# Optimization experiments

Hardware: AMD Instinct MI355X
Metric: run time of the kernel (lower is better)

The kernel has to match this reference:

```python
import jax, jax.numpy as jnp
import numpy as np

B, S, HID = 2, 2048, 2048
NH = 16
QLR, KVLR = 1536, 512
DN, DR, DV = 128, 64, 128          # qk_nope_head_dim, qk_rope_head_dim, v_head_dim
DQK = DN + DR                      # 192
SCALE = DQK ** -0.5
EPS = 1e-6


def rmsnorm(x, w):
    return x * jax.lax.rsqrt(jnp.mean(x * x, axis=-1, keepdims=True) + EPS) * w


def rotate_half(x):
    h = x.shape[-1] // 2
    return jnp.concatenate([-x[..., h:], x[..., :h]], axis=-1)


def setup_inputs() -> dict:
    key = jax.random.key(0)
    k = jax.random.split(key, 8)
    hidden_states = jax.random.normal(k[0], (B, S, HID), jnp.float32)
    # additive causal mask [B,1,S,S]
    causal = jnp.tril(jnp.ones((S, S), bool))
    attention_mask = jnp.where(causal, 0.0, -1e9).astype(jnp.float32)[None, None]
    attention_mask = jnp.broadcast_to(attention_mask, (B, 1, S, S))
    # RoPE tables for the rope head dim
    inv_freq = 1.0 / (10000.0 ** (jnp.arange(0, DR, 2, dtype=jnp.float32) / DR))
    t = jnp.arange(S, dtype=jnp.float32)[:, None] * inv_freq[None, :]
    emb = jnp.concatenate([t, t], axis=-1)        # [S, DR]
    cos, sin = jnp.cos(emb), jnp.sin(emb)
    s = 0.02
    w_qa = jax.random.normal(k[1], (HID, QLR), jnp.float32) * s
    qa_ln = jnp.ones((QLR,), jnp.float32)
    w_qb = jax.random.normal(k[2], (QLR, NH * DQK), jnp.float32) * s
    w_kva = jax.random.normal(k[3], (HID, KVLR + DR), jnp.float32) * s
    kva_ln = jnp.ones((KVLR,), jnp.float32)
    w_kvb = jax.random.normal(k[4], (KVLR, NH * (DN + DV)), jnp.float32) * s
    w_o = jax.random.normal(k[5], (NH * DV, HID), jnp.float32) * s
    return {"hidden_states": hidden_states, "attention_mask": attention_mask,
            "cos": cos, "sin": sin, "w_qa": w_qa, "qa_ln": qa_ln, "w_qb": w_qb,
            "w_kva": w_kva, "kva_ln": kva_ln, "w_kvb": w_kvb, "w_o": w_o}


def reference(hidden_states, attention_mask, cos, sin, w_qa, qa_ln, w_qb,
              w_kva, kva_ln, w_kvb, w_o):
    b, s, _ = hidden_states.shape
    # q low-rank path: q_b_proj(q_a_layernorm(q_a_proj(x)))
    q = rmsnorm(hidden_states @ w_qa, qa_ln) @ w_qb            # [B,S,NH*DQK]
    q = q.reshape(b, s, NH, DQK).transpose(0, 2, 1, 3)          # [B,NH,S,DQK]
    q_nope, q_pe = q[..., :DN], q[..., DN:]
    # compressed kv + shared rope key
    ckv = hidden_states @ w_kva                                 # [B,S,KVLR+DR]
    k_c, k_pe = ckv[..., :KVLR], ckv[..., KVLR:]
    kv = rmsnorm(k_c, kva_ln) @ w_kvb                           # [B,S,NH*(DN+DV)]
    kv = kv.reshape(b, s, NH, DN + DV).transpose(0, 2, 1, 3)    # [B,NH,S,DN+DV]
    k_nope, value_states = kv[..., :DN], kv[..., DN:]
    # RoPE on rope dims (k_pe is MQA: one head)
    k_pe = k_pe.reshape(b, 1, s, DR)
    c = cos[None, None]  # [1,1,S,DR]
    si = sin[None, None]
    q_pe = q_pe * c + rotate_half(q_pe) * si
    k_pe = k_pe * c + rotate_half(k_pe) * si
    k_pe = jnp.broadcast_to(k_pe, (b, NH, s, DR))
    query_states = jnp.concatenate([q_nope, q_pe], axis=-1)     # [B,NH,S,DQK]
    key_states = jnp.concatenate([k_nope, k_pe], axis=-1)       # [B,NH,S,DQK]
    attn_weights = jnp.einsum('bhqd,bhkd->bhqk', query_states, key_states) * SCALE
    attn_weights = attn_weights + attention_mask
    attn_probs = jax.nn.softmax(attn_weights.astype(jnp.float32), axis=-1)
    attn_probs = attn_probs.astype(value_states.dtype)
    attn_output = jnp.einsum('bhqk,bhkd->bhqd', attn_probs, value_states)
    attn_output = attn_output.transpose(0, 2, 1, 3).reshape(b, s, NH * DV)
    return attn_output @ w_o                                    # [B,S,HID]
```

## Files before the change

kernel.cpp:

```cpp
#include <hip/hip_runtime.h>
#include <type_traits>

typedef __attribute__((ext_vector_type(8))) short  vshort8;
typedef __attribute__((ext_vector_type(8))) __bf16 vbf16x8;
typedef __attribute__((ext_vector_type(4))) float  vfloat4;

__device__ __forceinline__ float bf2f(unsigned short h) {
    return __uint_as_float(((unsigned int)h) << 16);
}
__device__ __forceinline__ unsigned short f2bf(float f) {
    unsigned int u = __float_as_uint(f);
    unsigned int r = (u + 0x7FFFu + ((u >> 16) & 1u)) >> 16;
    return (unsigned short)r;
}
__device__ __forceinline__ vshort8 cvt8(const float* p) {
    float4 a = *(const float4*)p;
    float4 b = *(const float4*)(p + 4);
    vshort8 r;
    r[0] = (short)f2bf(a.x); r[1] = (short)f2bf(a.y);
    r[2] = (short)f2bf(a.z); r[3] = (short)f2bf(a.w);
    r[4] = (short)f2bf(b.x); r[5] = (short)f2bf(b.y);
    r[6] = (short)f2bf(b.z); r[7] = (short)f2bf(b.w);
    return r;
}
__device__ __forceinline__ void gload16(const void* g, void* lds) {
    __builtin_amdgcn_global_load_lds(
        (const __attribute__((address_space(1))) unsigned int*)g,
        (__attribute__((address_space(3))) unsigned int*)lds, 16, 0, 0);
}

__global__ __launch_bounds__(256) void hconv_kernel(
    const float* __restrict__ in, unsigned short* __restrict__ out, int n8)
{
    int i = blockIdx.x * 256 + threadIdx.x;
    if (i < n8) *(vshort8*)(out + (size_t)i * 8) = cvt8(in + (size_t)i * 8);
}

__global__ __launch_bounds__(256) void wtrans_kernel(
    const float* __restrict__ W, unsigned short* __restrict__ Wt,
    int ldw, int ldt, int rowoff)
{
    __shared__ __align__(16) unsigned short Ls[64][72];
    const int t = threadIdx.x;
    const int n0 = blockIdx.x * 64, k0 = blockIdx.y * 64;
    const int rr = t >> 2, cc = t & 3;

    const float* src = W + (size_t)(k0 + rr) * ldw + n0 + cc * 16;
    *(vshort8*)&Ls[rr][cc * 16]     = cvt8(src);
    *(vshort8*)&Ls[rr][cc * 16 + 8] = cvt8(src + 8);
    __syncthreads();

    unsigned short* dst = Wt + (size_t)(rowoff + n0 + rr) * ldt + k0 + cc * 16;
    vshort8 v0, v1;
    #pragma unroll
    for (int j = 0; j < 8; ++j) {
        v0[j] = (short)Ls[cc * 16 + j][rr];
        v1[j] = (short)Ls[cc * 16 + 8 + j][rr];
    }
    *(vshort8*)dst = v0;
    *(vshort8*)(dst + 8) = v1;
}

template<typename CT>
__global__ __launch_bounds__(256) void gemm_tt(
    const unsigned short* __restrict__ A, const unsigned short* __restrict__ Bt,
    CT* __restrict__ C0, CT* __restrict__ C1,
    int K, int N, int nsplit, int ldc0, int ldc1)
{
    __shared__ __align__(16) unsigned short As[128 * 32];
    __shared__ __align__(16) unsigned short Bs[128 * 32];

    const int t = threadIdx.x, lane = t & 63, w = t >> 6;
    const int lm = lane & 15, quad = lane >> 4;
    const int wm = w >> 1, wn = w & 1;
    const int m0 = blockIdx.y * 128, n0 = blockIdx.x * 128;
    const int srow = lane >> 2, sseg = lane & 3;

    vfloat4 acc[4][4] = {};

    for (int k0 = 0; k0 < K; k0 += 32) {
        #pragma unroll
        for (int j = 0; j < 2; ++j) {
            int r = w * 32 + j * 16 + srow;
            gload16(A  + (size_t)(m0 + r) * K + k0 + sseg * 8, &As[(w * 2 + j) * 512]);
            gload16(Bt + (size_t)(n0 + r) * K + k0 + sseg * 8, &Bs[(w * 2 + j) * 512]);
        }
        __syncthreads();

        vbf16x8 af[4], bw[4];
        #pragma unroll
        for (int i = 0; i < 4; ++i) {
            af[i] = *(const vbf16x8*)&As[(wm * 64 + i * 16 + lm) * 32 + quad * 8];
            bw[i] = *(const vbf16x8*)&Bs[(wn * 64 + i * 16 + lm) * 32 + quad * 8];
        }
        #pragma unroll
        for (int mi = 0; mi < 4; ++mi)
            #pragma unroll
            for (int ni = 0; ni < 4; ++ni)
                acc[mi][ni] = __builtin_amdgcn_mfma_f32_16x16x32_bf16(af[mi], bw[ni], acc[mi][ni], 0, 0, 0);
        __syncthreads();
    }

    #pragma unroll
    for (int mi = 0; mi < 4; ++mi) {
        #pragma unroll
        for (int ni = 0; ni < 4; ++ni) {
            int col = n0 + wn * 64 + ni * 16 + lm;
            if (col >= N) continue;
            #pragma unroll
            for (int r = 0; r < 4; ++r) {
                int row = m0 + wm * 64 + mi * 16 + quad * 4 + r;
                float v = acc[mi][ni][r];
                if (col < nsplit) {
                    if constexpr (std::is_same_v<CT, float>) C0[(size_t)row * ldc0 + col] = v;
                    else C0[(size_t)row * ldc0 + col] = f2bf(v);
                } else {
                    if constexpr (std::is_same_v<CT, float>) C1[(size_t)row * ldc1 + col - nsplit] = v;
                    else C1[(size_t)row * ldc1 + col - nsplit] = f2bf(v);
                }
            }
        }
    }
}

__global__ __launch_bounds__(256) void gemm_kv(
    const unsigned short* __restrict__ A, const unsigned short* __restrict__ Bt,
    unsigned short* __restrict__ Kn, unsigned short* __restrict__ VT, int K)
{
    __shared__ __align__(16) unsigned short As[128 * 32];
    __shared__ __align__(16) unsigned short Bs[128 * 32];

    const int t = threadIdx.x, lane = t & 63, w = t >> 6;
    const int lm = lane & 15, quad = lane >> 4;
    const int wm = w >> 1, wn = w & 1;
    const int m0 = blockIdx.y * 128, n0 = blockIdx.x * 128;
    const int srow = lane >> 2, sseg = lane & 3;

    vfloat4 acc[4][4] = {};

    for (int k0 = 0; k0 < K; k0 += 32) {
        #pragma unroll
        for (int j = 0; j < 2; ++j) {
            int r = w * 32 + j * 16 + srow;
            gload16(A  + (size_t)(m0 + r) * K + k0 + sseg * 8, &As[(w * 2 + j) * 512]);
            gload16(Bt + (size_t)(n0 + r) * K + k0 + sseg * 8, &Bs[(w * 2 + j) * 512]);
        }
        __syncthreads();

        vbf16x8 af[4], bw[4];
        #pragma unroll
        for (int i = 0; i < 4; ++i) {
            af[i] = *(const vbf16x8*)&As[(wm * 64 + i * 16 + lm) * 32 + quad * 8];
            bw[i] = *(const vbf16x8*)&Bs[(wn * 64 + i * 16 + lm) * 32 + quad * 8];
        }
        #pragma unroll
        for (int mi = 0; mi < 4; ++mi)
            #pragma unroll
            for (int ni = 0; ni < 4; ++ni)
                acc[mi][ni] = __builtin_amdgcn_mfma_f32_16x16x32_bf16(af[mi], bw[ni], acc[mi][ni], 0, 0, 0);
        __syncthreads();
    }

    #pragma unroll
    for (int mi = 0; mi < 4; ++mi) {
        #pragma unroll
        for (int ni = 0; ni < 4; ++ni) {
            int col = n0 + wn * 64 + ni * 16 + lm;
            int h = col >> 8, d = col & 255;
            #pragma unroll
            for (int r = 0; r < 4; ++r) {
                int row = m0 + wm * 64 + mi * 16 + quad * 4 + r;
                float v = acc[mi][ni][r];
                if (d < 128) {
                    Kn[(size_t)row * 2048 + h * 128 + d] = f2bf(v);
                } else {
                    int b = row >> 11, tok = row & 2047;
                    VT[((size_t)(b * 16 + h) * 128 + d - 128) * 2048 + tok] = f2bf(v);
                }
            }
        }
    }
}

__global__ __launch_bounds__(256) void rmsnorm_kernel(
    const unsigned short* __restrict__ in, const float* __restrict__ wgt,
    unsigned short* __restrict__ out, int width, int ld_in, int ld_out)
{
    const int row = blockIdx.x;
    const int t = threadIdx.x;
    const unsigned short* x = in + (size_t)row * ld_in;

    float ss = 0.f;
    for (int i = t; i < width; i += 256) { float v = bf2f(x[i]); ss += v * v; }
    #pragma unroll
    for (int off = 32; off > 0; off >>= 1) ss += __shfl_down(ss, off, 64);

    __shared__ float red[4];
    __shared__ float rr;
    if ((t & 63) == 0) red[t >> 6] = ss;
    __syncthreads();
    if (t == 0) rr = rsqrtf((red[0] + red[1] + red[2] + red[3]) / (float)width + 1e-6f);
    __syncthreads();
    float r = rr;
    unsigned short* o = out + (size_t)row * ld_out;
    for (int i = t; i < width; i += 256) o[i] = f2bf(bf2f(x[i]) * r * wgt[i]);
}

__global__ __launch_bounds__(256) void rope_q_kernel(
    unsigned short* __restrict__ q, const float* __restrict__ cosb,
    const float* __restrict__ sinb)
{
    const int row = blockIdx.x;
    const int s = row & 2047;
    const int t = threadIdx.x;
    unsigned short* qr = q + (size_t)row * 3072;
    const float SCALE = 0.07216878364870323f;

    for (int c = t; c < 3072; c += 256) {
        int d = c % 192;
        if (d < 128) {
            qr[c] = f2bf(bf2f(qr[c]) * SCALE);
        } else if (d < 160) {
            int i = d - 128;
            float cs = cosb[s * 64 + i];
            float sn = sinb[s * 64 + i];
            float x = bf2f(qr[c]);
            float y = bf2f(qr[c + 32]);
            qr[c]      = f2bf((x * cs - y * sn) * SCALE);
            qr[c + 32] = f2bf((y * cs + x * sn) * SCALE);
        }
    }
}

__global__ __launch_bounds__(64) void rope_k_kernel(
    const unsigned short* __restrict__ ckv, const float* __restrict__ cosb,
    const float* __restrict__ sinb, unsigned short* __restrict__ kpe)
{
    const int row = blockIdx.x;
    const int s = row & 2047;
    const int t = threadIdx.x;
    if (t < 32) {
        float cs = cosb[s * 64 + t];
        float sn = sinb[s * 64 + t];
        float x = bf2f(ckv[(size_t)row * 576 + 512 + t]);
        float y = bf2f(ckv[(size_t)row * 576 + 544 + t]);
        kpe[(size_t)row * 64 + t]      = f2bf(x * cs - y * sn);
        kpe[(size_t)row * 64 + 32 + t] = f2bf(y * cs + x * sn);
    }
}

__global__ __launch_bounds__(256) void flash_kernel(
    const unsigned short* __restrict__ Q, const unsigned short* __restrict__ Kn,
    const unsigned short* __restrict__ KPE, const unsigned short* __restrict__ VT,
    unsigned short* __restrict__ O)
{
    __shared__ __align__(16) unsigned short Ks[64][200];
    __shared__ __align__(16) unsigned short Vs[128][72];
    __shared__ __align__(16) unsigned short Ps[4][16][72];

    const int t    = threadIdx.x;
    const int lane = t & 63;
    const int w    = t >> 6;
    const int lm   = lane & 15, quad = lane >> 4;
    const int h = blockIdx.y, b = blockIdx.z;
    const int tb = b * 2048;
    const unsigned short* VTbh = VT + (size_t)(b * 16 + h) * 128 * 2048;

    for (int pi = 0; pi < 2; ++pi) {
        const int qt = pi ? (31 - blockIdx.x) : blockIdx.x;

        const int qtok = tb + qt * 64 + w * 16 + lm;
        vbf16x8 aq[6];
        #pragma unroll
        for (int ch = 0; ch < 6; ++ch)
            aq[ch] = *(const vbf16x8*)(Q + (size_t)qtok * 3072 + h * 192 + ch * 32 + quad * 8);

        vfloat4 acc_o[8];
        #pragma unroll
        for (int i = 0; i < 8; ++i) acc_o[i] = (vfloat4){0, 0, 0, 0};
        float mrow[4], lrow[4];
        #pragma unroll
        for (int r = 0; r < 4; ++r) { mrow[r] = -3.0e38f; lrow[r] = 0.f; }

        for (int kt = 0; kt <= qt; ++kt) {
            const int kb = kt * 64;
            #pragma unroll
            for (int it = 0; it < 4; ++it) {
                int idx = t + it * 256;
                int row = idx >> 4, sg = idx & 15;
                *(vshort8*)&Ks[row][sg * 8] =
                    *(const vshort8*)(Kn + (size_t)(tb + kb + row) * 2048 + h * 128 + sg * 8);
            }
            #pragma unroll
            for (int it = 0; it < 2; ++it) {
                int idx = t + it * 256;
                int row = idx >> 3, sg = idx & 7;
                *(vshort8*)&Ks[row][128 + sg * 8] =
                    *(const vshort8*)(KPE + (size_t)(tb + kb + row) * 64 + sg * 8);
            }
            #pragma unroll
            for (int it = 0; it < 4; ++it) {
                int idx = t + it * 256;
                int d = idx >> 3, sg = idx & 7;
                *(vshort8*)&Vs[d][sg * 8] =
                    *(const vshort8*)(VTbh + (size_t)d * 2048 + kb + sg * 8);
            }
            __syncthreads();

            vfloat4 accs[4];
            #pragma unroll
            for (int ni = 0; ni < 4; ++ni) accs[ni] = (vfloat4){0, 0, 0, 0};
            #pragma unroll
            for (int ni = 0; ni < 4; ++ni) {
                #pragma unroll
                for (int ch = 0; ch < 6; ++ch) {
                    vbf16x8 bk = *(const vbf16x8*)&Ks[ni * 16 + lm][ch * 32 + quad * 8];
                    accs[ni] = __builtin_amdgcn_mfma_f32_16x16x32_bf16(aq[ch], bk, accs[ni], 0, 0, 0);
                }
            }

            const int qrow = qt * 64 + w * 16 + quad * 4;
            #pragma unroll
            for (int ni = 0; ni < 4; ++ni) {
                int ki = kb + ni * 16 + lm;
                #pragma unroll
                for (int r = 0; r < 4; ++r)
                    if (ki > qrow + r) accs[ni][r] = -3.0e38f;
            }

            #pragma unroll
            for (int r = 0; r < 4; ++r) {
                float mx = fmaxf(fmaxf(accs[0][r], accs[1][r]), fmaxf(accs[2][r], accs[3][r]));
                #pragma unroll
                for (int off = 1; off < 16; off <<= 1) mx = fmaxf(mx, __shfl_xor(mx, off, 64));
                float mnew  = fmaxf(mrow[r], mx);
                float alpha = __expf(mrow[r] - mnew);
                float sum = 0.f;
                #pragma unroll
                for (int ni = 0; ni < 4; ++ni) {
                    float pv = __expf(accs[ni][r] - mnew);
                    accs[ni][r] = pv;
                    sum += pv;
                }
                #pragma unroll
                for (int off = 1; off < 16; off <<= 1) sum += __shfl_xor(sum, off, 64);
                lrow[r] = lrow[r] * alpha + sum;
                mrow[r] = mnew;
                #pragma unroll
                for (int vt = 0; vt < 8; ++vt) acc_o[vt][r] *= alpha;
            }

            #pragma unroll
            for (int ni = 0; ni < 4; ++ni)
                #pragma unroll
                for (int r = 0; r < 4; ++r)
                    Ps[w][quad * 4 + r][ni * 16 + lm] = f2bf(accs[ni][r]);
            __syncthreads();

            #pragma unroll
            for (int kc = 0; kc < 2; ++kc) {
                vbf16x8 ap = *(const vbf16x8*)&Ps[w][lm][kc * 32 + quad * 8];
                #pragma unroll
                for (int vt = 0; vt < 8; ++vt) {
                    vbf16x8 bv = *(const vbf16x8*)&Vs[vt * 16 + lm][kc * 32 + quad * 8];
                    acc_o[vt] = __builtin_amdgcn_mfma_f32_16x16x32_bf16(ap, bv, acc_o[vt], 0, 0, 0);
                }
            }
            __syncthreads();
        }

        #pragma unroll
        for (int r = 0; r < 4; ++r) {
            float inv = 1.f / lrow[r];
            int tok = tb + qt * 64 + w * 16 + quad * 4 + r;
            #pragma unroll
            for (int vt = 0; vt < 8; ++vt)
                O[(size_t)tok * 2048 + h * 128 + vt * 16 + lm] = f2bf(acc_o[vt][r] * inv);
        }
    }
}

extern "C" void kernel_launch(void* const* d_in, const int* in_sizes, int n_in,
                              void* d_out, int out_size, void* d_ws, size_t ws_size,
                              hipStream_t stream) {
    const float* hidden = (const float*)d_in[0];
    const float* cosb   = (const float*)d_in[2];
    const float* sinb   = (const float*)d_in[3];
    const float* w_qa   = (const float*)d_in[4];
    const float* qa_ln  = (const float*)d_in[5];
    const float* w_qb   = (const float*)d_in[6];
    const float* w_kva  = (const float*)d_in[7];
    const float* kva_ln = (const float*)d_in[8];
    const float* w_kvb  = (const float*)d_in[9];
    const float* w_o    = (const float*)d_in[10];
    float* out = (float*)d_out;

    unsigned short* ws   = (unsigned short*)d_ws;
    unsigned short* hb   = ws;
    unsigned short* Kn   = ws;
    unsigned short* wt12 = ws + 8388608;
    unsigned short* VT   = ws + 8388608;
    unsigned short* ot   = ws + 8388608;
    unsigned short* qbuf = ws + 16777216;
    unsigned short* q_a  = ws + 29360128;
    unsigned short* ckv  = ws + 35651584;
    unsigned short* aout = ws + 29360128;
    unsigned short* qbt  = ws + 38010880;
    unsigned short* kvbt = ws + 42729472;
    unsigned short* kvn  = ws + 44826624;
    unsigned short* kpe  = ws + 46923776;

    dim3 blk(256);

    hconv_kernel<<<4096, blk, 0, stream>>>(hidden, hb, 1048576);
    wtrans_kernel<<<dim3(24, 32), blk, 0, stream>>>(w_qa,  wt12, 1536, 2048, 0);
    wtrans_kernel<<<dim3( 9, 32), blk, 0, stream>>>(w_kva, wt12,  576, 2048, 1536);
    wtrans_kernel<<<dim3(48, 24), blk, 0, stream>>>(w_qb,  qbt,  3072, 1536, 0);
    wtrans_kernel<<<dim3(64,  8), blk, 0, stream>>>(w_kvb, kvbt, 4096,  512, 0);

    gemm_tt<unsigned short><<<dim3(17, 32), blk, 0, stream>>>(
        hb, wt12, q_a, ckv, 2048, 2112, 1536, 1536, 576);

    rmsnorm_kernel<<<4096, blk, 0, stream>>>(q_a, qa_ln, q_a, 1536, 1536, 1536);
    rmsnorm_kernel<<<4096, blk, 0, stream>>>(ckv, kva_ln, kvn, 512, 576, 512);
    rope_k_kernel<<<4096, dim3(64), 0, stream>>>(ckv, cosb, sinb, kpe);

    gemm_tt<unsigned short><<<dim3(24, 32), blk, 0, stream>>>(
        q_a, qbt, qbuf, qbuf, 1536, 3072, 3072, 3072, 3072);
    rope_q_kernel<<<4096, blk, 0, stream>>>(qbuf, cosb, sinb);

    gemm_kv<<<dim3(32, 32), blk, 0, stream>>>(kvn, kvbt, Kn, VT, 512);

    flash_kernel<<<dim3(16, 16, 2), blk, 0, stream>>>(qbuf, Kn, kpe, VT, aout);

    wtrans_kernel<<<dim3(32, 32), blk, 0, stream>>>(w_o, ot, 2048, 2048, 0);

    gemm_tt<float><<<dim3(16, 32), blk, 0, stream>>>(
        aout, ot, out, out, 2048, 2048, 2048, 2048, 2048);
}
```

Before: 560.9 us.

## Prefetch next K/V tile into registers and launch one q-tile per block

The flash attention kernel now loads the next K, rope-K and V tile into registers while computing the current tile, then writes them to shared memory after the PV step, overlapping global loads with MFMA work. The paired-q-tile loop per block is replaced by one q-tile per block, with a doubled grid and heaviest tiles scheduled first. The causal mask is applied only on the diagonal tile, and launch bounds request 3 blocks per SM. This adds register pressure and an extra barrier per iteration, and balances load through hardware scheduling instead of manual pairing.

```diff
diff --git a/kernel.cpp b/kernel.cpp
--- a/kernel.cpp
+++ b/kernel.cpp
@@ -249,7 +249,7 @@
     }
 }
 
-__global__ __launch_bounds__(256) void flash_kernel(
+__global__ __launch_bounds__(256, 3) void flash_kernel(
     const unsigned short* __restrict__ Q, const unsigned short* __restrict__ Kn,
     const unsigned short* __restrict__ KPE, const unsigned short* __restrict__ VT,
     unsigned short* __restrict__ O)
@@ -265,60 +265,90 @@
     const int h = blockIdx.y, b = blockIdx.z;
     const int tb = b * 2048;
     const unsigned short* VTbh = VT + (size_t)(b * 16 + h) * 128 * 2048;
-
-    for (int pi = 0; pi < 2; ++pi) {
-        const int qt = pi ? (31 - blockIdx.x) : blockIdx.x;
-
-        const int qtok = tb + qt * 64 + w * 16 + lm;
-        vbf16x8 aq[6];
-        #pragma unroll
-        for (int ch = 0; ch < 6; ++ch)
-            aq[ch] = *(const vbf16x8*)(Q + (size_t)qtok * 3072 + h * 192 + ch * 32 + quad * 8);
-
-        vfloat4 acc_o[8];
-        #pragma unroll
-        for (int i = 0; i < 8; ++i) acc_o[i] = (vfloat4){0, 0, 0, 0};
-        float mrow[4], lrow[4];
-        #pragma unroll
-        for (int r = 0; r < 4; ++r) { mrow[r] = -3.0e38f; lrow[r] = 0.f; }
-
-        for (int kt = 0; kt <= qt; ++kt) {
-            const int kb = kt * 64;
+    const int qt = 31 - (int)blockIdx.x;
+
+    const int qtok = tb + qt * 64 + w * 16 + lm;
+    vbf16x8 aq[6];
+    #pragma unroll
+    for (int ch = 0; ch < 6; ++ch)
+        aq[ch] = *(const vbf16x8*)(Q + (size_t)qtok * 3072 + h * 192 + ch * 32 + quad * 8);
+
+    vfloat4 acc_o[8];
+    #pragma unroll
+    for (int i = 0; i < 8; ++i) acc_o[i] = (vfloat4){0, 0, 0, 0};
+    float mrow[4], lrow[4];
+    #pragma unroll
+    for (int r = 0; r < 4; ++r) { mrow[r] = -3.0e38f; lrow[r] = 0.f; }
+
+    vshort8 rk[4], rp[2], rv[4];
+
+    #pragma unroll
+    for (int it = 0; it < 4; ++it) {
+        int idx = t + it * 256, row = idx >> 4, sg = idx & 15;
+        rk[it] = *(const vshort8*)(Kn + (size_t)(tb + row) * 2048 + h * 128 + sg * 8);
+    }
+    #pragma unroll
+    for (int it = 0; it < 2; ++it) {
+        int idx = t + it * 256, row = idx >> 3, sg = idx & 7;
+        rp[it] = *(const vshort8*)(KPE + (size_t)(tb + row) * 64 + sg * 8);
+    }
+    #pragma unroll
+    for (int it = 0; it < 4; ++it) {
+        int idx = t + it * 256, d = idx >> 3, sg = idx & 7;
+        rv[it] = *(const vshort8*)(VTbh + (size_t)d * 2048 + sg * 8);
+    }
+    #pragma unroll
+    for (int it = 0; it < 4; ++it) {
+        int idx = t + it * 256, row = idx >> 4, sg = idx & 15;
+        *(vshort8*)&Ks[row][sg * 8] = rk[it];
+    }
+    #pragma unroll
+    for (int it = 0; it < 2; ++it) {
+        int idx = t + it * 256, row = idx >> 3, sg = idx & 7;
+        *(vshort8*)&Ks[row][128 + sg * 8] = rp[it];
+    }
+    #pragma unroll
+    for (int it = 0; it < 4; ++it) {
+        int idx = t + it * 256, d = idx >> 3, sg = idx & 7;
+        *(vshort8*)&Vs[d][sg * 8] = rv[it];
+    }
+    __syncthreads();
+
+    for (int kt = 0; kt <= qt; ++kt) {
+        const int kb = kt * 64;
+
+        if (kt < qt) {
+            const int nb = kb + 64;
             #pragma unroll
             for (int it = 0; it < 4; ++it) {
-                int idx = t + it * 256;
-                int row = idx >> 4, sg = idx & 15;
-                *(vshort8*)&Ks[row][sg * 8] =
-                    *(const vshort8*)(Kn + (size_t)(tb + kb + row) * 2048 + h * 128 + sg * 8);
+                int idx = t + it * 256, row = idx >> 4, sg = idx & 15;
+                rk[it] = *(const vshort8*)(Kn + (size_t)(tb + nb + row) * 2048 + h * 128 + sg * 8);
             }
             #pragma unroll
             for (int it = 0; it < 2; ++it) {
-                int idx = t + it * 256;
-                int row = idx >> 3, sg = idx & 7;
-                *(vshort8*)&Ks[row][128 + sg * 8] =
-                    *(const vshort8*)(KPE + (size_t)(tb + kb + row) * 64 + sg * 8);
+                int idx = t + it * 256, row = idx >> 3, sg = idx & 7;
+                rp[it] = *(const vshort8*)(KPE + (size_t)(tb + nb + row) * 64 + sg * 8);
             }
             #pragma unroll
             for (int it = 0; it < 4; ++it) {
-                int idx = t + it * 256;
-                int d = idx >> 3, sg = idx & 7;
-                *(vshort8*)&Vs[d][sg * 8] =
-                    *(const vshort8*)(VTbh + (size_t)d * 2048 + kb + sg * 8);
-            }
-            __syncthreads();
-
-            vfloat4 accs[4];
-            #pragma unroll
-            for (int ni = 0; ni < 4; ++ni) accs[ni] = (vfloat4){0, 0, 0, 0};
-            #pragma unroll
-            for (int ni = 0; ni < 4; ++ni) {
-                #pragma unroll
-                for (int ch = 0; ch < 6; ++ch) {
-                    vbf16x8 bk = *(const vbf16x8*)&Ks[ni * 16 + lm][ch * 32 + quad * 8];
-                    accs[ni] = __builtin_amdgcn_mfma_f32_16x16x32_bf16(aq[ch], bk, accs[ni], 0, 0, 0);
-                }
-            }
-
+                int idx = t + it * 256, d = idx >> 3, sg = idx & 7;
+                rv[it] = *(const vshort8*)(VTbh + (size_t)d * 2048 + nb + sg * 8);
+            }
+        }
+
+        vfloat4 accs[4];
+        #pragma unroll
+        for (int ni = 0; ni < 4; ++ni) accs[ni] = (vfloat4){0, 0, 0, 0};
+        #pragma unroll
+        for (int ni = 0; ni < 4; ++ni) {
+            #pragma unroll
+            for (int ch = 0; ch < 6; ++ch) {
+                vbf16x8 bk = *(const vbf16x8*)&Ks[ni * 16 + lm][ch * 32 + quad * 8];
+                accs[ni] = __builtin_amdgcn_mfma_f32_16x16x32_bf16(aq[ch], bk, accs[ni], 0, 0, 0);
+            }
+        }
+
+        if (kt == qt) {
             const int qrow = qt * 64 + w * 16 + quad * 4;
             #pragma unroll
             for (int ni = 0; ni < 4; ++ni) {
@@ -327,56 +357,75 @@
                 for (int r = 0; r < 4; ++r)
                     if (ki > qrow + r) accs[ni][r] = -3.0e38f;
             }
-
-            #pragma unroll
-            for (int r = 0; r < 4; ++r) {
-                float mx = fmaxf(fmaxf(accs[0][r], accs[1][r]), fmaxf(accs[2][r], accs[3][r]));
-                #pragma unroll
-                for (int off = 1; off < 16; off <<= 1) mx = fmaxf(mx, __shfl_xor(mx, off, 64));
-                float mnew  = fmaxf(mrow[r], mx);
-                float alpha = __expf(mrow[r] - mnew);
-                float sum = 0.f;
-                #pragma unroll
-                for (int ni = 0; ni < 4; ++ni) {
-                    float pv = __expf(accs[ni][r] - mnew);
-                    accs[ni][r] = pv;
-                    sum += pv;
-                }
-                #pragma unroll
-                for (int off = 1; off < 16; off <<= 1) sum += __shfl_xor(sum, off, 64);
-                lrow[r] = lrow[r] * alpha + sum;
-                mrow[r] = mnew;
-                #pragma unroll
-                for (int vt = 0; vt < 8; ++vt) acc_o[vt][r] *= alpha;
-            }
-
-            #pragma unroll
-            for (int ni = 0; ni < 4; ++ni)
-                #pragma unroll
-                for (int r = 0; r < 4; ++r)
-                    Ps[w][quad * 4 + r][ni * 16 + lm] = f2bf(accs[ni][r]);
+        }
+
+        #pragma unroll
+        for (int r = 0; r < 4; ++r) {
+            float mx = fmaxf(fmaxf(accs[0][r], accs[1][r]), fmaxf(accs[2][r], accs[3][r]));
+            #pragma unroll
+            for (int off = 1; off < 16; off <<= 1) mx = fmaxf(mx, __shfl_xor(mx, off, 64));
+            float mnew  = fmaxf(mrow[r], mx);
+            float alpha = __expf(mrow[r] - mnew);
+            float sum = 0.f;
+            #pragma unroll
+            for (int ni = 0; ni < 4; ++ni) {
+                float pv = __expf(accs[ni][r] - mnew);
+                accs[ni][r] = pv;
+                sum += pv;
+            }
+            #pragma unroll
+            for (int off = 1; off < 16; off <<= 1) sum += __shfl_xor(sum, off, 64);
+            lrow[r] = lrow[r] * alpha + sum;
+            mrow[r] = mnew;
+            #pragma unroll
+            for (int vt = 0; vt < 8; ++vt) acc_o[vt][r] *= alpha;
+        }
+
+        #pragma unroll
+        for (int ni = 0; ni < 4; ++ni)
+            #pragma unroll
+            for (int r = 0; r < 4; ++r)
+                Ps[w][quad * 4 + r][ni * 16 + lm] = f2bf(accs[ni][r]);
+        __syncthreads();
+
+        #pragma unroll
+        for (int kc = 0; kc < 2; ++kc) {
+            vbf16x8 ap = *(const vbf16x8*)&Ps[w][lm][kc * 32 + quad * 8];
+            #pragma unroll
+            for (int vt = 0; vt < 8; ++vt) {
+                vbf16x8 bv = *(const vbf16x8*)&Vs[vt * 16 + lm][kc * 32 + quad * 8];
+                acc_o[vt] = __builtin_amdgcn_mfma_f32_16x16x32_bf16(ap, bv, acc_o[vt], 0, 0, 0);
+            }
+        }
+        __syncthreads();
+
+        if (kt < qt) {
+            #pragma unroll
+            for (int it = 0; it < 4; ++it) {
+                int idx = t + it * 256, row = idx >> 4, sg = idx & 15;
+                *(vshort8*)&Ks[row][sg * 8] = rk[it];
+            }
+            #pragma unroll
+            for (int it = 0; it < 2; ++it) {
+                int idx = t + it * 256, row = idx >> 3, sg = idx & 7;
+                *(vshort8*)&Ks[row][128 + sg * 8] = rp[it];
+            }
+            #pragma unroll
+            for (int it = 0; it < 4; ++it) {
+                int idx = t + it * 256, d = idx >> 3, sg = idx & 7;
+                *(vshort8*)&Vs[d][sg * 8] = rv[it];
+            }
             __syncthreads();
-
-            #pragma unroll
-            for (int kc = 0; kc < 2; ++kc) {
-                vbf16x8 ap = *(const vbf16x8*)&Ps[w][lm][kc * 32 + quad * 8];
-                #pragma unroll
-                for (int vt = 0; vt < 8; ++vt) {
-                    vbf16x8 bv = *(const vbf16x8*)&Vs[vt * 16 + lm][kc * 32 + quad * 8];
-                    acc_o[vt] = __builtin_amdgcn_mfma_f32_16x16x32_bf16(ap, bv, acc_o[vt], 0, 0, 0);
-                }
-            }
-            __syncthreads();
-        }
-
-        #pragma unroll
-        for (int r = 0; r < 4; ++r) {
-            float inv = 1.f / lrow[r];
-            int tok = tb + qt * 64 + w * 16 + quad * 4 + r;
-            #pragma unroll
-            for (int vt = 0; vt < 8; ++vt)
-                O[(size_t)tok * 2048 + h * 128 + vt * 16 + lm] = f2bf(acc_o[vt][r] * inv);
-        }
+        }
+    }
+
+    #pragma unroll
+    for (int r = 0; r < 4; ++r) {
+        float inv = 1.f / lrow[r];
+        int tok = tb + qt * 64 + w * 16 + quad * 4 + r;
+        #pragma unroll
+        for (int vt = 0; vt < 8; ++vt)
+            O[(size_t)tok * 2048 + h * 128 + vt * 16 + lm] = f2bf(acc_o[vt][r] * inv);
     }
 }
 
@@ -431,7 +480,7 @@
 
     gemm_kv<<<dim3(32, 32), blk, 0, stream>>>(kvn, kvbt, Kn, VT, 512);
 
-    flash_kernel<<<dim3(16, 16, 2), blk, 0, stream>>>(qbuf, Kn, kpe, VT, aout);
+    flash_kernel<<<dim3(32, 16, 2), blk, 0, stream>>>(qbuf, Kn, kpe, VT, aout);
 
     wtrans_kernel<<<dim3(32, 32), blk, 0, stream>>>(w_o, ot, 2048, 2048, 0);
 
```

After: 654.9 us. +16.7%, slower.
